# Kernel tuning notes

Measured on AMD Instinct MI355X. Metric: run time of the kernel, lower is better.

The kernel has to match this reference:

```python
import jax, jax.numpy as jnp
import numpy as np

NEG = -10000.0
START_TAG = 62
STOP_TAG = 63


def setup_inputs() -> dict:
    key = jax.random.key(0)
    k1, k2, k3 = jax.random.split(key, 3)
    S, B, T = 512, 512, 64
    feats = jax.random.normal(k1, (S, B, T), dtype=jnp.float32)
    tags = jax.random.randint(k2, (S, B), 0, START_TAG, dtype=jnp.int32)
    mask = jnp.ones((S, B), dtype=jnp.float32)
    # nn.Parameter(torch.randn(T,T)) with start row / stop col clamped to -1e4
    transitions = jax.random.normal(k3, (T, T), dtype=jnp.float32)
    transitions = transitions.at[START_TAG, :].set(NEG).at[:, STOP_TAG].set(NEG)
    return {"feats": feats, "tags": tags, "mask": mask, "transitions": transitions}


def _score_sentence(feats, tags, mask, transitions):
    # feats: [S,B,T], tags/mask: [S,B]
    S, B, T = feats.shape
    emission = jnp.take_along_axis(feats, tags[:, :, None], axis=2)[..., 0]  # [S,B]
    start = jnp.full((1, B), START_TAG, dtype=tags.dtype)
    tags_ext = jnp.concatenate([start, tags], axis=0)  # [S+1,B]
    trans = transitions[tags_ext[:-1], tags_ext[1:]]  # [S,B]
    score = jnp.sum((emission + trans) * mask, axis=0)  # [B]
    last_idx = mask.sum(axis=0).astype(jnp.int32) - 1  # [B]
    last_tags = tags[last_idx, jnp.arange(B)]
    return score + transitions[last_tags, STOP_TAG]


def _forward_alg(feats, mask, transitions):
    S, B, T = feats.shape
    log_alpha0 = jnp.full((B, T), NEG, dtype=feats.dtype).at[:, START_TAG].set(0.0)

    def step(log_alpha, xs):
        f_i, m_i = xs  # [B,T], [B]
        # broadcast: [B, prev_tag, next_tag]
        scores = log_alpha[:, :, None] + transitions[None, :, :] + f_i[:, None, :]
        nxt = jax.nn.logsumexp(scores, axis=1)  # [B,T]
        log_alpha = jnp.where(m_i[:, None] > 0, nxt, log_alpha)
        return log_alpha, None

    log_alpha, _ = jax.lax.scan(step, log_alpha0, (feats, mask))
    return jax.nn.logsumexp(log_alpha + transitions[STOP_TAG][None, :], axis=1)  # [B]


def reference(feats, tags, mask, transitions):
    score_true = _score_sentence(feats, tags, mask, transitions)
    log_z = _forward_alg(feats, mask, transitions)
    return jnp.mean(log_z - score_true)
```

## Files before the change

kernel.cpp:

```cpp
#include <hip/hip_runtime.h>

#define NEG (-10000.0f)
#define START_TAG 62
#define STOP_TAG 63
#define SLEN 512
#define BATCH 512
#define NTAG 64

__global__ __launch_bounds__(64) __attribute__((amdgpu_waves_per_eu(1, 1)))
void crf_fwd(const float* __restrict__ feats,
             const int* __restrict__ tags,
             const float* __restrict__ mask,
             const float* __restrict__ trans,
             float* __restrict__ diff ) {
    const int b = blockIdx.x;
    const int j = threadIdx.x;

    __shared__ float smask[SLEN];

    float e[NTAG];
    float colsum = 0.0f;
#pragma unroll
    for (int i = 0; i < NTAG; ++i) {
        e[i] = __expf(trans[i * NTAG + j]);
        colsum += e[i];
    }
    const float tstop = trans[STOP_TAG * NTAG + j];

    float mreg[8];
#pragma unroll
    for (int k = 0; k < 8; ++k)
        mreg[k] = mask[(64 * k + j) * BATCH + b];

#pragma unroll
    for (int k = 0; k < 8; ++k)
        smask[64 * k + j] = mreg[k];

    float f_s0 = feats[(0 * BATCH + b) * NTAG + j];
    float m0 = __uint_as_float(__builtin_amdgcn_readlane(__float_as_uint(mreg[0]), 0));
    float alpha = (m0 > 0.0f) ? (NEG + log1pf(colsum) + f_s0)
                              : ((j == START_TAG) ? 0.0f : NEG);

    if (j == 0) smask[0] = 0.0f;
    __syncthreads();

    const float* fp = feats + (size_t)b * NTAG + j;
    float fr[8];
#pragma unroll
    for (int t = 0; t < 8; ++t)
        fr[t] = fp[(size_t)t * BATCH * NTAG];

    for (int blk = 0; blk < 64; ++blk) {
#pragma unroll
        for (int t = 0; t < 8; ++t) {
            const int s = blk * 8 + t;
            const float fc = fr[t];
            int sp = s + 8;
            if (sp > SLEN - 1) sp = SLEN - 1;
            fr[t] = fp[(size_t)sp * BATCH * NTAG];

            const float mk = smask[s];

            float C = __uint_as_float(
                __builtin_amdgcn_readfirstlane(__float_as_uint(alpha)));
            float p = __expf(alpha - C);

            unsigned pu = __float_as_uint(p);
            float a0 = 0.0f, a1 = 0.0f, a2 = 0.0f, a3 = 0.0f;
#pragma unroll
            for (int i = 0; i < NTAG; i += 4) {
                a0 = fmaf(__uint_as_float(__builtin_amdgcn_readlane(pu, i + 0)), e[i + 0], a0);
                a1 = fmaf(__uint_as_float(__builtin_amdgcn_readlane(pu, i + 1)), e[i + 1], a1);
                a2 = fmaf(__uint_as_float(__builtin_amdgcn_readlane(pu, i + 2)), e[i + 2], a2);
                a3 = fmaf(__uint_as_float(__builtin_amdgcn_readlane(pu, i + 3)), e[i + 3], a3);
            }
            float acc = (a0 + a1) + (a2 + a3);

            float nxt = C + __logf(acc) + fc;
            alpha = (mk > 0.0f) ? nxt : alpha;
        }
    }

    float v = alpha + tstop;
    float m2 = v;
#pragma unroll
    for (int w = 32; w >= 1; w >>= 1)
        m2 = fmaxf(m2, __shfl_xor(m2, w, 64));
    float pe = __expf(v - m2);
#pragma unroll
    for (int w = 32; w >= 1; w >>= 1)
        pe += __shfl_xor(pe, w, 64);
    float logz = m2 + __logf(pe);

    float psc = 0.0f, pms = 0.0f;
#pragma unroll
    for (int k = 0; k < 8; ++k) {
        int s = j + 64 * k;
        int tg = tags[s * BATCH + b];
        float mk = mreg[k];
        int tprev = (s == 0) ? START_TAG : tags[(s - 1) * BATCH + b];
        float em = feats[((size_t)s * BATCH + b) * NTAG + tg];
        psc = fmaf(em + trans[tprev * NTAG + tg], mk, psc);
        pms += mk;
    }
#pragma unroll
    for (int w = 32; w >= 1; w >>= 1) {
        psc += __shfl_xor(psc, w, 64);
        pms += __shfl_xor(pms, w, 64);
    }

    if (j == 0) {
        int last_idx = (int)(pms + 0.5f) - 1;
        int ltag = tags[last_idx * BATCH + b];
        float score = psc + trans[ltag * NTAG + STOP_TAG];
        diff[b] = logz - score;
    }
}

__global__ __launch_bounds__(512) void crf_reduce(const float* __restrict__ diff,
                                                  float* __restrict__ out) {
    __shared__ float sdata[8];
    int t = threadIdx.x;
    float val = diff[t];
#pragma unroll
    for (int w = 32; w >= 1; w >>= 1)
        val += __shfl_xor(val, w, 64);
    if ((t & 63) == 0) sdata[t >> 6] = val;
    __syncthreads();
    if (t == 0) {
        float ssum = 0.0f;
        for (int i = 0; i < 8; ++i) ssum += sdata[i];
        out[0] = ssum * (1.0f / (float)BATCH);
    }
}

extern "C" void kernel_launch(void* const* d_in, const int* in_sizes, int n_in,
                              void* d_out, int out_size, void* d_ws, size_t ws_size,
                              hipStream_t stream) {
    const float* feats = (const float*)d_in[0];
    const int* tags = (const int*)d_in[1];
    const float* mask = (const float*)d_in[2];
    const float* trans = (const float*)d_in[3];
    float* out = (float*)d_out;
    float* diff = (float*)d_ws;

    crf_fwd<<<BATCH, 64, 0, stream>>>(feats, tags, mask, trans, diff);
    crf_reduce<<<1, 512, 0, stream>>>(diff, out);
}
```

Measured before the change: 237.0 us.

## Process two batch elements per wavefront to interleave independent recurrences

Each 64-thread block now advances two independent CRF forward recurrences (batch elements 2b and 2b+1) together, interleaving their readlane/FMA chains and sharing the exp-transition registers. The grid shrinks to 256 blocks. The goal is to hide the serial dependency latency of the single-chain loop through instruction-level parallelism. In exchange, register pressure roughly doubles for the feature prefetch buffers, and with 256 blocks fewer wavefronts run across the CUs.

```diff
diff --git a/kernel.cpp b/kernel.cpp
--- a/kernel.cpp
+++ b/kernel.cpp
@@ -13,10 +13,12 @@
              const float* __restrict__ mask,
              const float* __restrict__ trans,
              float* __restrict__ diff ) {
-    const int b = blockIdx.x;
+    const int bp = blockIdx.x;
+    const int bA = 2 * bp;
+    const int bB = 2 * bp + 1;
     const int j = threadIdx.x;
 
-    __shared__ float smask[SLEN];
+    __shared__ float2 smask[SLEN];
 
     float e[NTAG];
     float colsum = 0.0f;
@@ -27,93 +29,122 @@
     }
     const float tstop = trans[STOP_TAG * NTAG + j];
 
-    float mreg[8];
+    float mra[8], mrb[8];
 #pragma unroll
-    for (int k = 0; k < 8; ++k)
-        mreg[k] = mask[(64 * k + j) * BATCH + b];
+    for (int k = 0; k < 8; ++k) {
+        mra[k] = mask[(64 * k + j) * BATCH + bA];
+        mrb[k] = mask[(64 * k + j) * BATCH + bB];
+    }
 
 #pragma unroll
     for (int k = 0; k < 8; ++k)
-        smask[64 * k + j] = mreg[k];
+        smask[64 * k + j] = make_float2(mra[k], mrb[k]);
 
-    float f_s0 = feats[(0 * BATCH + b) * NTAG + j];
-    float m0 = __uint_as_float(__builtin_amdgcn_readlane(__float_as_uint(mreg[0]), 0));
-    float alpha = (m0 > 0.0f) ? (NEG + log1pf(colsum) + f_s0)
-                              : ((j == START_TAG) ? 0.0f : NEG);
+    float fA0 = feats[(0 * BATCH + bA) * NTAG + j];
+    float fB0 = feats[(0 * BATCH + bB) * NTAG + j];
+    float m0A = __uint_as_float(__builtin_amdgcn_readlane(__float_as_uint(mra[0]), 0));
+    float m0B = __uint_as_float(__builtin_amdgcn_readlane(__float_as_uint(mrb[0]), 0));
+    float init_cold = (j == START_TAG) ? 0.0f : NEG;
+    float alphaA = (m0A > 0.0f) ? (NEG + log1pf(colsum) + fA0) : init_cold;
+    float alphaB = (m0B > 0.0f) ? (NEG + log1pf(colsum) + fB0) : init_cold;
 
-    if (j == 0) smask[0] = 0.0f;
+    if (j == 0) smask[0] = make_float2(0.0f, 0.0f);
     __syncthreads();
 
-    const float* fp = feats + (size_t)b * NTAG + j;
-    float fr[8];
+    const float* fpA = feats + (size_t)bA * NTAG + j;
+    const float* fpB = feats + (size_t)bB * NTAG + j;
+    float frA[8], frB[8];
 #pragma unroll
-    for (int t = 0; t < 8; ++t)
-        fr[t] = fp[(size_t)t * BATCH * NTAG];
+    for (int t = 0; t < 8; ++t) {
+        frA[t] = fpA[(size_t)t * BATCH * NTAG];
+        frB[t] = fpB[(size_t)t * BATCH * NTAG];
+    }
 
     for (int blk = 0; blk < 64; ++blk) {
 #pragma unroll
         for (int t = 0; t < 8; ++t) {
             const int s = blk * 8 + t;
-            const float fc = fr[t];
+            const float fcA = frA[t];
+            const float fcB = frB[t];
             int sp = s + 8;
             if (sp > SLEN - 1) sp = SLEN - 1;
-            fr[t] = fp[(size_t)sp * BATCH * NTAG];
+            frA[t] = fpA[(size_t)sp * BATCH * NTAG];
+            frB[t] = fpB[(size_t)sp * BATCH * NTAG];
 
-            const float mk = smask[s];
+            const float2 mk2 = smask[s];
 
-            float C = __uint_as_float(
-                __builtin_amdgcn_readfirstlane(__float_as_uint(alpha)));
-            float p = __expf(alpha - C);
+            float CA = __uint_as_float(
+                __builtin_amdgcn_readfirstlane(__float_as_uint(alphaA)));
+            float CB = __uint_as_float(
+                __builtin_amdgcn_readfirstlane(__float_as_uint(alphaB)));
+            float pA = __expf(alphaA - CA);
+            float pB = __expf(alphaB - CB);
 
-            unsigned pu = __float_as_uint(p);
+            unsigned puA = __float_as_uint(pA);
+            unsigned puB = __float_as_uint(pB);
             float a0 = 0.0f, a1 = 0.0f, a2 = 0.0f, a3 = 0.0f;
+            float b0 = 0.0f, b1 = 0.0f, b2 = 0.0f, b3 = 0.0f;
 #pragma unroll
             for (int i = 0; i < NTAG; i += 4) {
-                a0 = fmaf(__uint_as_float(__builtin_amdgcn_readlane(pu, i + 0)), e[i + 0], a0);
-                a1 = fmaf(__uint_as_float(__builtin_amdgcn_readlane(pu, i + 1)), e[i + 1], a1);
-                a2 = fmaf(__uint_as_float(__builtin_amdgcn_readlane(pu, i + 2)), e[i + 2], a2);
-                a3 = fmaf(__uint_as_float(__builtin_amdgcn_readlane(pu, i + 3)), e[i + 3], a3);
+                a0 = fmaf(__uint_as_float(__builtin_amdgcn_readlane(puA, i + 0)), e[i + 0], a0);
+                b0 = fmaf(__uint_as_float(__builtin_amdgcn_readlane(puB, i + 0)), e[i + 0], b0);
+                a1 = fmaf(__uint_as_float(__builtin_amdgcn_readlane(puA, i + 1)), e[i + 1], a1);
+                b1 = fmaf(__uint_as_float(__builtin_amdgcn_readlane(puB, i + 1)), e[i + 1], b1);
+                a2 = fmaf(__uint_as_float(__builtin_amdgcn_readlane(puA, i + 2)), e[i + 2], a2);
+                b2 = fmaf(__uint_as_float(__builtin_amdgcn_readlane(puB, i + 2)), e[i + 2], b2);
+                a3 = fmaf(__uint_as_float(__builtin_amdgcn_readlane(puA, i + 3)), e[i + 3], a3);
+                b3 = fmaf(__uint_as_float(__builtin_amdgcn_readlane(puB, i + 3)), e[i + 3], b3);
             }
-            float acc = (a0 + a1) + (a2 + a3);
+            float accA = (a0 + a1) + (a2 + a3);
+            float accB = (b0 + b1) + (b2 + b3);
 
-            float nxt = C + __logf(acc) + fc;
-            alpha = (mk > 0.0f) ? nxt : alpha;
+            float nxtA = CA + __logf(accA) + fcA;
+            float nxtB = CB + __logf(accB) + fcB;
+            alphaA = (mk2.x > 0.0f) ? nxtA : alphaA;
+            alphaB = (mk2.y > 0.0f) ? nxtB : alphaB;
         }
     }
 
-    float v = alpha + tstop;
-    float m2 = v;
+    float logzAB[2];
 #pragma unroll
-    for (int w = 32; w >= 1; w >>= 1)
-        m2 = fmaxf(m2, __shfl_xor(m2, w, 64));
-    float pe = __expf(v - m2);
+    for (int bb = 0; bb < 2; ++bb) {
+        float v = ((bb == 0) ? alphaA : alphaB) + tstop;
+        float m2 = v;
 #pragma unroll
-    for (int w = 32; w >= 1; w >>= 1)
-        pe += __shfl_xor(pe, w, 64);
-    float logz = m2 + __logf(pe);
-
-    float psc = 0.0f, pms = 0.0f;
+        for (int w = 32; w >= 1; w >>= 1)
+            m2 = fmaxf(m2, __shfl_xor(m2, w, 64));
+        float pe = __expf(v - m2);
 #pragma unroll
-    for (int k = 0; k < 8; ++k) {
-        int s = j + 64 * k;
-        int tg = tags[s * BATCH + b];
-        float mk = mreg[k];
-        int tprev = (s == 0) ? START_TAG : tags[(s - 1) * BATCH + b];
-        float em = feats[((size_t)s * BATCH + b) * NTAG + tg];
-        psc = fmaf(em + trans[tprev * NTAG + tg], mk, psc);
-        pms += mk;
-    }
-#pragma unroll
-    for (int w = 32; w >= 1; w >>= 1) {
-        psc += __shfl_xor(psc, w, 64);
-        pms += __shfl_xor(pms, w, 64);
+        for (int w = 32; w >= 1; w >>= 1)
+            pe += __shfl_xor(pe, w, 64);
+        logzAB[bb] = m2 + __logf(pe);
     }
 
-    if (j == 0) {
-        int last_idx = (int)(pms + 0.5f) - 1;
-        int ltag = tags[last_idx * BATCH + b];
-        float score = psc + trans[ltag * NTAG + STOP_TAG];
-        diff[b] = logz - score;
+#pragma unroll
+    for (int bb = 0; bb < 2; ++bb) {
+        const int bcur = 2 * bp + bb;
+        float psc = 0.0f, pms = 0.0f;
+#pragma unroll
+        for (int k = 0; k < 8; ++k) {
+            int s = j + 64 * k;
+            int tg = tags[s * BATCH + bcur];
+            float mk = (bb == 0) ? mra[k] : mrb[k];
+            int tprev = (s == 0) ? START_TAG : tags[(s - 1) * BATCH + bcur];
+            float em = feats[((size_t)s * BATCH + bcur) * NTAG + tg];
+            psc = fmaf(em + trans[tprev * NTAG + tg], mk, psc);
+            pms += mk;
+        }
+#pragma unroll
+        for (int w = 32; w >= 1; w >>= 1) {
+            psc += __shfl_xor(psc, w, 64);
+            pms += __shfl_xor(pms, w, 64);
+        }
+        if (j == 0) {
+            int last_idx = (int)(pms + 0.5f) - 1;
+            int ltag = tags[last_idx * BATCH + bcur];
+            float score = psc + trans[ltag * NTAG + STOP_TAG];
+            diff[bcur] = logzAB[bb] - score;
+        }
     }
 }
 
@@ -144,6 +175,6 @@
     float* out = (float*)d_out;
     float* diff = (float*)d_ws;
 
-    crf_fwd<<<BATCH, 64, 0, stream>>>(feats, tags, mask, trans, diff);
+    crf_fwd<<<BATCH / 2, 64, 0, stream>>>(feats, tags, mask, trans, diff);
     crf_reduce<<<1, 512, 0, stream>>>(diff, out);
 }
```

Result: slower. 334.8 us (+41.3%).

## Run CRF forward recursion in linear space with power-of-two rescaling

Applied to the files above, without the earlier changes.

The log-space recurrence (readfirstlane max, exp, log per step) is replaced by a linear-domain recurrence on exp(alpha). Each step is rescaled by a power-of-two factor taken from the exponent bits of lane 0's sum, and the accumulated exponents are added back as ln2 terms at the end. The 64 readlane broadcasts per step give way to a double-buffered LDS vector that every lane reads with packed float2 FMAs. This removes one log per step and the SGPR broadcast chain, at the cost of an LDS round trip and an implicit wave-level ordering between steps, plus some risk of underflow or overflow for lanes far from lane 0.

```diff
diff --git a/kernel.cpp b/kernel.cpp
--- a/kernel.cpp
+++ b/kernel.cpp
@@ -6,6 +6,13 @@
 #define SLEN 512
 #define BATCH 512
 #define NTAG 64
+
+typedef float f32x2 __attribute__((ext_vector_type(2)));
+typedef float f32x4 __attribute__((ext_vector_type(4)));
+
+__device__ __forceinline__ float readlane_f(float v, int lane) {
+    return __uint_as_float(__builtin_amdgcn_readlane(__float_as_uint(v), lane));
+}
 
 __global__ __launch_bounds__(64) __attribute__((amdgpu_waves_per_eu(1, 1)))
 void crf_fwd(const float* __restrict__ feats,
@@ -17,80 +24,96 @@
     const int j = threadIdx.x;
 
     __shared__ float smask[SLEN];
+    __shared__ __align__(16) float qraw[2][NTAG];
 
-    float e[NTAG];
+    f32x2 e2[32];
     float colsum = 0.0f;
 #pragma unroll
-    for (int i = 0; i < NTAG; ++i) {
-        e[i] = __expf(trans[i * NTAG + j]);
-        colsum += e[i];
+    for (int r = 0; r < 32; ++r) {
+        float lo = __expf(trans[(2 * r) * NTAG + j]);
+        float hi = __expf(trans[(2 * r + 1) * NTAG + j]);
+        e2[r] = (f32x2){lo, hi};
+        colsum += lo + hi;
     }
     const float tstop = trans[STOP_TAG * NTAG + j];
 
     float mreg[8];
 #pragma unroll
-    for (int k = 0; k < 8; ++k)
-        mreg[k] = mask[(64 * k + j) * BATCH + b];
-
+    for (int k = 0; k < 8; ++k) mreg[k] = mask[(64 * k + j) * BATCH + b];
 #pragma unroll
-    for (int k = 0; k < 8; ++k)
-        smask[64 * k + j] = mreg[k];
+    for (int k = 0; k < 8; ++k) smask[64 * k + j] = mreg[k];
 
     float f_s0 = feats[(0 * BATCH + b) * NTAG + j];
-    float m0 = __uint_as_float(__builtin_amdgcn_readlane(__float_as_uint(mreg[0]), 0));
-    float alpha = (m0 > 0.0f) ? (NEG + log1pf(colsum) + f_s0)
-                              : ((j == START_TAG) ? 0.0f : NEG);
+    float m0 = readlane_f(mreg[0], 0);
+    float alpha0 = (m0 > 0.0f) ? (NEG + log1pf(colsum) + f_s0)
+                               : ((j == START_TAG) ? 0.0f : NEG);
+    const float C0 = readlane_f(alpha0, START_TAG);
+    float q = __expf(alpha0 - C0);
 
     if (j == 0) smask[0] = 0.0f;
+    qraw[0][j] = q;
     __syncthreads();
 
     const float* fp = feats + (size_t)b * NTAG + j;
     float fr[8];
 #pragma unroll
-    for (int t = 0; t < 8; ++t)
-        fr[t] = fp[(size_t)t * BATCH * NTAG];
+    for (int t = 0; t < 8; ++t) fr[t] = fp[(size_t)t * BATCH * NTAG];
+
+    float rinv = 1.0f;
+    int kcur = 0;
+    int ktot = 0;
 
     for (int blk = 0; blk < 64; ++blk) {
 #pragma unroll
         for (int t = 0; t < 8; ++t) {
             const int s = blk * 8 + t;
-            const float fc = fr[t];
+            const int ph = t & 1;
+
+            const float mk = smask[s];
+
+            float ef = __expf(fr[t]);
             int sp = s + 8;
             if (sp > SLEN - 1) sp = SLEN - 1;
             fr[t] = fp[(size_t)sp * BATCH * NTAG];
+            float efr = ef * rinv;
 
-            const float mk = smask[s];
+            const f32x4* qv = (const f32x4*)(&qraw[ph][0]);
+            f32x2 acc[8];
+#pragma unroll
+            for (int c = 0; c < 8; ++c) acc[c] = (f32x2){0.0f, 0.0f};
+#pragma unroll
+            for (int r = 0; r < 16; ++r) {
+                f32x4 q4 = qv[r];
+                f32x2 qlo = (f32x2){q4.x, q4.y};
+                f32x2 qhi = (f32x2){q4.z, q4.w};
+                acc[(2 * r) & 7] = qlo * e2[2 * r] + acc[(2 * r) & 7];
+                acc[(2 * r + 1) & 7] = qhi * e2[2 * r + 1] + acc[(2 * r + 1) & 7];
+            }
+            f32x2 s01 = (acc[0] + acc[1]) + (acc[2] + acc[3]);
+            f32x2 s23 = (acc[4] + acc[5]) + (acc[6] + acc[7]);
+            f32x2 sall = s01 + s23;
+            float acc_s = sall.x + sall.y;
 
-            float C = __uint_as_float(
-                __builtin_amdgcn_readfirstlane(__float_as_uint(alpha)));
-            float p = __expf(alpha - C);
+            float qn = acc_s * efr;
+            bool upd = (mk > 0.0f);
+            q = upd ? qn : q;
+            qraw[ph ^ 1][j] = q;
 
-            unsigned pu = __float_as_uint(p);
-            float a0 = 0.0f, a1 = 0.0f, a2 = 0.0f, a3 = 0.0f;
-#pragma unroll
-            for (int i = 0; i < NTAG; i += 4) {
-                a0 = fmaf(__uint_as_float(__builtin_amdgcn_readlane(pu, i + 0)), e[i + 0], a0);
-                a1 = fmaf(__uint_as_float(__builtin_amdgcn_readlane(pu, i + 1)), e[i + 1], a1);
-                a2 = fmaf(__uint_as_float(__builtin_amdgcn_readlane(pu, i + 2)), e[i + 2], a2);
-                a3 = fmaf(__uint_as_float(__builtin_amdgcn_readlane(pu, i + 3)), e[i + 3], a3);
-            }
-            float acc = (a0 + a1) + (a2 + a3);
-
-            float nxt = C + __logf(acc) + fc;
-            alpha = (mk > 0.0f) ? nxt : alpha;
+            ktot = upd ? (ktot + kcur) : ktot;
+            unsigned a0u = __builtin_amdgcn_readfirstlane(__float_as_uint(acc_s));
+            int ke = (int)((a0u >> 23) & 0xffu) - 127;
+            ke = (ke < -60) ? -60 : ((ke > 60) ? 60 : ke);
+            float rnew = __uint_as_float((unsigned)(127 - ke) << 23);
+            rinv = upd ? rnew : rinv;
+            kcur = upd ? ke : kcur;
         }
     }
 
-    float v = alpha + tstop;
-    float m2 = v;
+    float et = __expf(tstop);
+    float pe = q * et;
 #pragma unroll
-    for (int w = 32; w >= 1; w >>= 1)
-        m2 = fmaxf(m2, __shfl_xor(m2, w, 64));
-    float pe = __expf(v - m2);
-#pragma unroll
-    for (int w = 32; w >= 1; w >>= 1)
-        pe += __shfl_xor(pe, w, 64);
-    float logz = m2 + __logf(pe);
+    for (int w = 32; w >= 1; w >>= 1) pe += __shfl_xor(pe, w, 64);
+    float logz = __logf(pe) + C0 + (float)ktot * 0.6931471805599453f;
 
     float psc = 0.0f, pms = 0.0f;
 #pragma unroll
```

Result: faster. 199.0 us (-16.0%).
